# Kernel optimization log

Measured on AMD Instinct MI355X. Metric: run time of the kernel, lower is better.

The kernel has to match this reference:

```python
import jax, jax.numpy as jnp
import numpy as np

B, T = 32, 512
VOCAB, WDIM, H, NUM_LABELS = 100000, 300, 256, 2


def setup_inputs() -> dict:
    key = jax.random.key(0)
    ks = jax.random.split(key, 16)
    x = jax.random.randint(ks[0], (B, T), 0, VOCAB, dtype=jnp.int32)
    lengths = jax.random.randint(ks[1], (B,), T // 2, T + 1, dtype=jnp.int32)
    mask = (jnp.arange(T)[None, :] < lengths[:, None]).astype(jnp.int32)
    s = 0.05
    emb_table = jax.random.normal(ks[2], (VOCAB, WDIM), jnp.float32)
    W_in = jax.random.normal(ks[3], (WDIM, H), jnp.float32) * s
    b_in = jnp.zeros((H,), jnp.float32)
    Wih_f = jax.random.normal(ks[4], (H, 4 * H), jnp.float32) * s
    Whh_f = jax.random.normal(ks[5], (H, 4 * H), jnp.float32) * s
    bl_f = jnp.zeros((4 * H,), jnp.float32)
    Wih_b = jax.random.normal(ks[6], (H, 4 * H), jnp.float32) * s
    Whh_b = jax.random.normal(ks[7], (H, 4 * H), jnp.float32) * s
    bl_b = jnp.zeros((4 * H,), jnp.float32)
    Wfc = jax.random.normal(ks[8], (2 * H, H), jnp.float32) * s
    bfc = jnp.zeros((H,), jnp.float32)
    Wout = jax.random.normal(ks[9], (H, NUM_LABELS), jnp.float32) * s
    bout = jnp.zeros((NUM_LABELS,), jnp.float32)
    return dict(emb_table=emb_table, W_in=W_in, b_in=b_in,
                Wih_f=Wih_f, Whh_f=Whh_f, bl_f=bl_f,
                Wih_b=Wih_b, Whh_b=Whh_b, bl_b=bl_b,
                Wfc=Wfc, bfc=bfc, Wout=Wout, bout=bout,
                x=x, mask=mask, lengths=lengths)


def _lstm_dir(xs, maskf, Wih, Whh, b, reverse):
    # xs: [B,T,H], maskf: [B,T] float. Masked LSTM: padded steps carry state.
    xs_t = jnp.swapaxes(xs, 0, 1)                # [T,B,H]
    m_t = jnp.swapaxes(maskf, 0, 1)[..., None]   # [T,B,1]
    h0 = jnp.zeros((xs.shape[0], Whh.shape[0]), xs.dtype)
    c0 = h0

    def step(carry, inp):
        h, c = carry
        xt, mt = inp
        z = xt @ Wih + h @ Whh + b               # [B,4H]
        i, f, g, o = jnp.split(z, 4, axis=-1)
        i = jax.nn.sigmoid(i); f = jax.nn.sigmoid(f)
        g = jnp.tanh(g); o = jax.nn.sigmoid(o)
        c_new = f * c + i * g
        h_new = o * jnp.tanh(c_new)
        c = mt * c_new + (1.0 - mt) * c
        h = mt * h_new + (1.0 - mt) * h
        return (h, c), h

    _, hs = jax.lax.scan(step, (h0, c0), (xs_t, m_t), reverse=reverse)
    return jnp.swapaxes(hs, 0, 1)                # [B,T,H]


def reference(emb_table, W_in, b_in, Wih_f, Whh_f, bl_f, Wih_b, Whh_b, bl_b,
              Wfc, bfc, Wout, bout, x, mask, lengths):
    maskf = mask.astype(jnp.float32)
    x_vecs = jnp.take(emb_table, x, axis=0)          # [B,T,WDIM]
    z = jax.nn.relu(x_vecs @ W_in + b_in)            # wordvec layer + relu
    h_fwd = _lstm_dir(z, maskf, Wih_f, Whh_f, bl_f, reverse=False)
    h_bwd = _lstm_dir(z, maskf, Wih_b, Whh_b, bl_b, reverse=True)
    h_mat = jnp.concatenate([h_fwd, h_bwd], axis=-1)  # [B,T,2H]
    h_masked = h_mat * maskf[..., None]
    fc_in = jnp.sum(h_masked / lengths.astype(jnp.float32)[:, None, None], axis=1)
    fc_hidden = jax.nn.relu(fc_in @ Wfc + bfc)        # dropout = identity (eval)
    return fc_hidden @ Wout + bout                    # [B, NUM_LABELS]
```

## Files before the change

### kernel.cpp

```cpp
#include <hip/hip_runtime.h>
#include <math.h>

#define B_    32
#define T_    512
#define WDIM_ 300
#define H_    256
#define G4_   1024
#define M_    (B_ * T_)

#define NBG   16
#define NCG   4
#define NWG   128
#define THR   512
#define HXN   (2 * 2 * B_ * H_)

#define RPT4(M, b)  M(b) M((b)+1) M((b)+2) M((b)+3)
#define RPT16(M, b) RPT4(M, b) RPT4(M, (b)+4) RPT4(M, (b)+8) RPT4(M, (b)+12)
#define RPT64(M)    RPT16(M, 0) RPT16(M, 16) RPT16(M, 32) RPT16(M, 48)

__global__ __launch_bounds__(256)
void k_embed_proj(const float* __restrict__ emb, const float* __restrict__ Win,
                  const float* __restrict__ bin, const int* __restrict__ x,
                  float* __restrict__ z)
{
    __shared__ float Ash[16][132];
    __shared__ float Bsh[16][132];
    __shared__ int   rows[128];

    const int tid = threadIdx.x;
    const int tx = tid & 15, ty = tid >> 4;
    const int rm = blockIdx.y * 128;
    const int cn = blockIdx.x * 128;

    if (tid < 128) rows[tid] = x[rm + tid];
    __syncthreads();

    float acc[8][8];
#pragma unroll
    for (int i = 0; i < 8; ++i)
#pragma unroll
        for (int j = 0; j < 8; ++j) acc[i][j] = 0.f;

    for (int kc = 0; kc < 19; ++kc) {
        const int k0 = kc * 16;
#pragma unroll
        for (int e = 0; e < 8; ++e) {
            const int idx = e * 256 + tid;
            const int r = idx >> 4, kk = idx & 15;
            const int k = k0 + kk;
            const int v = rows[r];
            Ash[kk][r] = (k < WDIM_) ? emb[(size_t)v * WDIM_ + k] : 0.f;
        }
#pragma unroll
        for (int e = 0; e < 8; ++e) {
            const int idx = e * 256 + tid;
            const int kk = idx >> 7, n = idx & 127;
            const int k = k0 + kk;
            Bsh[kk][n] = (k < WDIM_) ? Win[(size_t)k * H_ + cn + n] : 0.f;
        }
        __syncthreads();
#pragma unroll
        for (int kk = 0; kk < 16; ++kk) {
            float a[8], bb[8];
#pragma unroll
            for (int i = 0; i < 8; ++i) a[i] = Ash[kk][ty * 8 + i];
#pragma unroll
            for (int j = 0; j < 8; ++j) bb[j] = Bsh[kk][tx * 8 + j];
#pragma unroll
            for (int i = 0; i < 8; ++i)
#pragma unroll
                for (int j = 0; j < 8; ++j) acc[i][j] += a[i] * bb[j];
        }
        __syncthreads();
    }

#pragma unroll
    for (int i = 0; i < 8; ++i) {
        const int row = rm + ty * 8 + i;
#pragma unroll
        for (int j = 0; j < 8; ++j) {
            const int col = cn + tx * 8 + j;
            z[(size_t)row * H_ + col] = fmaxf(acc[i][j] + bin[col], 0.f);
        }
    }
}

__global__ __launch_bounds__(256)
void k_in_proj(const float* __restrict__ z,
               const float* __restrict__ Wf, const float* __restrict__ blf,
               const float* __restrict__ Wb, const float* __restrict__ blb,
               float* __restrict__ Pf, float* __restrict__ Pb)
{
    const float* W  = blockIdx.z ? Wb  : Wf;
    const float* bl = blockIdx.z ? blb : blf;
    float*       P  = blockIdx.z ? Pb  : Pf;

    __shared__ float Ash[16][132];
    __shared__ float Bsh[16][132];

    const int tid = threadIdx.x;
    const int tx = tid & 15, ty = tid >> 4;
    const int rm = blockIdx.y * 128;
    const int cn = blockIdx.x * 128;

    float acc[8][8];
#pragma unroll
    for (int i = 0; i < 8; ++i)
#pragma unroll
        for (int j = 0; j < 8; ++j) acc[i][j] = 0.f;

    for (int kc = 0; kc < 16; ++kc) {
        const int k0 = kc * 16;
#pragma unroll
        for (int e = 0; e < 8; ++e) {
            const int idx = e * 256 + tid;
            const int r = idx >> 4, kk = idx & 15;
            Ash[kk][r] = z[(size_t)(rm + r) * H_ + k0 + kk];
        }
#pragma unroll
        for (int e = 0; e < 8; ++e) {
            const int idx = e * 256 + tid;
            const int kk = idx >> 7, n = idx & 127;
            Bsh[kk][n] = W[(size_t)(k0 + kk) * G4_ + cn + n];
        }
        __syncthreads();
#pragma unroll
        for (int kk = 0; kk < 16; ++kk) {
            float a[8], bb[8];
#pragma unroll
            for (int i = 0; i < 8; ++i) a[i] = Ash[kk][ty * 8 + i];
#pragma unroll
            for (int j = 0; j < 8; ++j) bb[j] = Bsh[kk][tx * 8 + j];
#pragma unroll
            for (int i = 0; i < 8; ++i)
#pragma unroll
                for (int j = 0; j < 8; ++j) acc[i][j] += a[i] * bb[j];
        }
        __syncthreads();
    }

#pragma unroll
    for (int i = 0; i < 8; ++i) {
        const int row = rm + ty * 8 + i;
#pragma unroll
        for (int j = 0; j < 8; ++j) {
            const int col = cn + tx * 8 + j;
            P[(size_t)row * G4_ + col] = acc[i][j] + bl[col];
        }
    }
}

__global__ void k_init(unsigned long long* __restrict__ hx)
{
    const int i = blockIdx.x * blockDim.x + threadIdx.x;
    if (i < HXN) hx[i] = 0ull;
}

__global__ __launch_bounds__(THR, 2)
void k_lstm_persist(const float* __restrict__ Pf, const float* __restrict__ Pb,
                    const float* __restrict__ Whf, const float* __restrict__ Whb,
                    const int* __restrict__ lengths,
                    unsigned long long* __restrict__ hx,
                    float* __restrict__ pool)
{
    __shared__ float h_sh[2][256];
    __shared__ float zp[4][2][256];

    const int tid = threadIdx.x;
    const int wg  = blockIdx.x;
    const int bg  = wg & 15;
    const int dir = (wg >> 4) & 1;
    const int cg  = wg >> 5;

    const float* P   = dir ? Pb  : Pf;
    const float* Whh = dir ? Whb : Whf;

    const int brow0 = bg * 2;
    const int len0 = lengths[brow0], len1 = lengths[brow0 + 1];
    const int tmax = max(len0, len1);

    const int q   = tid >> 7;
    const int c0  = (tid & 127) * 2;
    const int g0  = c0 >> 6;
    const int dd0 = c0 & 63;
    const int gcol0 = g0 * 256 + cg * 64 + dd0;
    const int q64 = q * 64;

    float2 wv[64];
    {
        const float* wp = Whh + (size_t)q64 * G4_ + gcol0;
#define LOADW(k) wv[k] = *(const float2*)(wp + (size_t)(k) * G4_);
        RPT64(LOADW)
#undef LOADW
    }

    const int gr    = tid >> 6;
    const int gdd   = tid & 63;
    const int gbrow = brow0 + gr;
    const int glen  = gr ? len1 : len0;
    float cst = 0.f, hreg = 0.f, pacc = 0.f;

    const int lrow = tid >> 8;
    const int ld   = tid & 255;
    unsigned long long* slotR = hx + ((size_t)dir * 32 + brow0 + lrow) * 256 + ld;
    unsigned long long* slotW = hx + ((size_t)dir * 32 + gbrow) * 256 + cg * 64 + gdd;
    const size_t bufStride = (size_t)2 * B_ * H_;

    for (int s = 0; s < tmax; ++s) {
        const int tt = dir ? (tmax - 1 - s) : s;

        float pv0 = 0.f, pv1 = 0.f, pv2 = 0.f, pv3 = 0.f;
        if (tid < 128) {
            const float* pr = P + (size_t)(gbrow * T_ + tt) * G4_ + cg * 64 + gdd;
            pv0 = pr[0]; pv1 = pr[256]; pv2 = pr[512]; pv3 = pr[768];
        }

        {
            const unsigned long long* sp = slotR + (size_t)(s & 1) * bufStride;
            unsigned long long pk = __hip_atomic_load(sp, __ATOMIC_RELAXED,
                                                      __HIP_MEMORY_SCOPE_AGENT);
            while ((unsigned)(pk >> 32) < (unsigned)s) {
                __builtin_amdgcn_s_sleep(1);
                pk = __hip_atomic_load(sp, __ATOMIC_RELAXED,
                                       __HIP_MEMORY_SCOPE_AGENT);
            }
            h_sh[lrow][ld] = __uint_as_float((unsigned)pk);
        }
        __syncthreads();

        {
            const float* h0 = &h_sh[0][q64];
            const float* h1 = &h_sh[1][q64];
            float a00 = 0.f, a01 = 0.f, a10 = 0.f, a11 = 0.f;
#define GEMV4(k4) { \
            const float4 hv0 = *(const float4*)(h0 + 4 * (k4)); \
            const float4 hv1 = *(const float4*)(h1 + 4 * (k4)); \
            a00 += hv0.x * wv[4*(k4)  ].x; a01 += hv0.x * wv[4*(k4)  ].y; \
            a10 += hv1.x * wv[4*(k4)  ].x; a11 += hv1.x * wv[4*(k4)  ].y; \
            a00 += hv0.y * wv[4*(k4)+1].x; a01 += hv0.y * wv[4*(k4)+1].y; \
            a10 += hv1.y * wv[4*(k4)+1].x; a11 += hv1.y * wv[4*(k4)+1].y; \
            a00 += hv0.z * wv[4*(k4)+2].x; a01 += hv0.z * wv[4*(k4)+2].y; \
            a10 += hv1.z * wv[4*(k4)+2].x; a11 += hv1.z * wv[4*(k4)+2].y; \
            a00 += hv0.w * wv[4*(k4)+3].x; a01 += hv0.w * wv[4*(k4)+3].y; \
            a10 += hv1.w * wv[4*(k4)+3].x; a11 += hv1.w * wv[4*(k4)+3].y; }
            RPT16(GEMV4, 0)
#undef GEMV4
            *(float2*)&zp[q][0][c0] = make_float2(a00, a01);
            *(float2*)&zp[q][1][c0] = make_float2(a10, a11);
        }
        __syncthreads();

        if (tid < 128) {
            const int ci = gdd;
            float zi = pv0 + zp[0][gr][ci]       + zp[1][gr][ci]       + zp[2][gr][ci]       + zp[3][gr][ci];
            float zf = pv1 + zp[0][gr][64 + ci]  + zp[1][gr][64 + ci]  + zp[2][gr][64 + ci]  + zp[3][gr][64 + ci];
            float zg = pv2 + zp[0][gr][128 + ci] + zp[1][gr][128 + ci] + zp[2][gr][128 + ci] + zp[3][gr][128 + ci];
            float zo = pv3 + zp[0][gr][192 + ci] + zp[1][gr][192 + ci] + zp[2][gr][192 + ci] + zp[3][gr][192 + ci];
            const float ig = 1.f / (1.f + expf(-zi));
            const float fg = 1.f / (1.f + expf(-zf));
            const float gg = tanhf(zg);
            const float og = 1.f / (1.f + expf(-zo));
            const float cn = fg * cst + ig * gg;
            const float hn = og * tanhf(cn);
            if (tt < glen) { cst = cn; hreg = hn; pacc += hn; }
            const unsigned long long opk =
                ((unsigned long long)(unsigned)(s + 1) << 32) |
                (unsigned long long)__float_as_uint(hreg);
            __hip_atomic_store(slotW + (size_t)((s + 1) & 1) * bufStride, opk,
                               __ATOMIC_RELAXED, __HIP_MEMORY_SCOPE_AGENT);
        }
    }

    if (tid < 128)
        pool[gbrow * 512 + dir * 256 + cg * 64 + gdd] = pacc / (float)glen;
}

__global__ __launch_bounds__(256)
void k_fc(const float* __restrict__ pool, const float* __restrict__ Wfc,
          const float* __restrict__ bfc, const float* __restrict__ Wout,
          const float* __restrict__ bout, float* __restrict__ out)
{
    __shared__ float p_sh[512];
    __shared__ float red[8];

    const int tid = threadIdx.x;
    const int b   = blockIdx.x;

    p_sh[tid]       = pool[b * 512 + tid];
    p_sh[256 + tid] = pool[b * 512 + 256 + tid];
    __syncthreads();

    float acc = bfc[tid];
#pragma unroll 8
    for (int k = 0; k < 512; ++k)
        acc += p_sh[k] * Wfc[(size_t)k * H_ + tid];
    const float fh = fmaxf(acc, 0.f);

    float p0 = fh * Wout[tid * 2 + 0];
    float p1 = fh * Wout[tid * 2 + 1];
#pragma unroll
    for (int off = 32; off > 0; off >>= 1) {
        p0 += __shfl_down(p0, off);
        p1 += __shfl_down(p1, off);
    }
    const int wave = tid >> 6;
    if ((tid & 63) == 0) { red[wave * 2] = p0; red[wave * 2 + 1] = p1; }
    __syncthreads();
    if (tid == 0) {
        out[b * 2 + 0] = red[0] + red[2] + red[4] + red[6] + bout[0];
        out[b * 2 + 1] = red[1] + red[3] + red[5] + red[7] + bout[1];
    }
}

__global__ void k_sentinel(float* out, int n)
{
    const int i = blockIdx.x * blockDim.x + threadIdx.x;
    if (i < n) out[i] = 1.0e9f;
}

extern "C" void kernel_launch(void* const* d_in, const int* in_sizes, int n_in,
                              void* d_out, int out_size, void* d_ws, size_t ws_size,
                              hipStream_t stream)
{
    const float* emb  = (const float*)d_in[0];
    const float* Win  = (const float*)d_in[1];
    const float* bin  = (const float*)d_in[2];
    const float* Wihf = (const float*)d_in[3];
    const float* Whhf = (const float*)d_in[4];
    const float* blf  = (const float*)d_in[5];
    const float* Wihb = (const float*)d_in[6];
    const float* Whhb = (const float*)d_in[7];
    const float* blb  = (const float*)d_in[8];
    const float* Wfc  = (const float*)d_in[9];
    const float* bfc  = (const float*)d_in[10];
    const float* Wout = (const float*)d_in[11];
    const float* bout = (const float*)d_in[12];
    const int*   x    = (const int*)d_in[13];
    const int*   lens = (const int*)d_in[15];
    float*       out  = (float*)d_out;

    const size_t need = ((size_t)M_ * H_ + 2 * (size_t)M_ * G4_) * sizeof(float);
    if (ws_size < need) {
        hipLaunchKernelGGL(k_sentinel, dim3(1), dim3(64), 0, stream, out, out_size);
        return;
    }

    float* z  = (float*)d_ws;
    float* Pf = z + (size_t)M_ * H_;
    float* Pb = Pf + (size_t)M_ * G4_;

    unsigned long long* hx   = (unsigned long long*)d_ws;
    float*              pool = (float*)(hx + HXN);

    hipLaunchKernelGGL(k_embed_proj, dim3(2, 128), dim3(256), 0, stream,
                       emb, Win, bin, x, z);
    hipLaunchKernelGGL(k_in_proj, dim3(8, 128, 2), dim3(256), 0, stream,
                       z, Wihf, blf, Wihb, blb, Pf, Pb);
    hipLaunchKernelGGL(k_init, dim3(128), dim3(256), 0, stream, hx);
    hipLaunchKernelGGL(k_lstm_persist, dim3(NWG), dim3(THR), 0, stream,
                       Pf, Pb, Whhf, Whhb, lens, hx, pool);
    hipLaunchKernelGGL(k_fc, dim3(32), dim3(256), 0, stream,
                       pool, Wfc, bfc, Wout, bout, out);
}
```

Baseline: 1.520 ms.

## Split LSTM hidden columns across 8 workgroups instead of 4

```diff
diff --git a/kernel.cpp b/kernel.cpp
--- a/kernel.cpp
+++ b/kernel.cpp
@@ -8,9 +8,8 @@
 #define G4_   1024
 #define M_    (B_ * T_)
 
-#define NBG   16
-#define NCG   4
-#define NWG   128
+#define NCG   8
+#define NWG   256
 #define THR   512
 #define HXN   (2 * 2 * B_ * H_)
 
@@ -164,7 +163,7 @@
                     float* __restrict__ pool)
 {
     __shared__ float h_sh[2][256];
-    __shared__ float zp[4][2][256];
+    __shared__ float zp[4][2][128];
 
     const int tid = threadIdx.x;
     const int wg  = blockIdx.x;
@@ -180,22 +179,22 @@
     const int tmax = max(len0, len1);
 
     const int q   = tid >> 7;
-    const int c0  = (tid & 127) * 2;
-    const int g0  = c0 >> 6;
-    const int dd0 = c0 & 63;
-    const int gcol0 = g0 * 256 + cg * 64 + dd0;
+    const int cl  = tid & 127;
+    const int g0  = cl >> 5;
+    const int dd0 = cl & 31;
+    const int gcol = g0 * 256 + cg * 32 + dd0;
     const int q64 = q * 64;
 
-    float2 wv[64];
+    float wv[64];
     {
-        const float* wp = Whh + (size_t)q64 * G4_ + gcol0;
-#define LOADW(k) wv[k] = *(const float2*)(wp + (size_t)(k) * G4_);
+        const float* wp = Whh + (size_t)q64 * G4_ + gcol;
+#define LOADW(k) wv[k] = wp[(size_t)(k) * G4_];
         RPT64(LOADW)
 #undef LOADW
     }
 
-    const int gr    = tid >> 6;
-    const int gdd   = tid & 63;
+    const int gr    = tid >> 5;
+    const int gd    = tid & 31;
     const int gbrow = brow0 + gr;
     const int glen  = gr ? len1 : len0;
     float cst = 0.f, hreg = 0.f, pacc = 0.f;
@@ -203,15 +202,15 @@
     const int lrow = tid >> 8;
     const int ld   = tid & 255;
     unsigned long long* slotR = hx + ((size_t)dir * 32 + brow0 + lrow) * 256 + ld;
-    unsigned long long* slotW = hx + ((size_t)dir * 32 + gbrow) * 256 + cg * 64 + gdd;
+    unsigned long long* slotW = hx + ((size_t)dir * 32 + gbrow) * 256 + cg * 32 + gd;
     const size_t bufStride = (size_t)2 * B_ * H_;
 
     for (int s = 0; s < tmax; ++s) {
         const int tt = dir ? (tmax - 1 - s) : s;
 
         float pv0 = 0.f, pv1 = 0.f, pv2 = 0.f, pv3 = 0.f;
-        if (tid < 128) {
-            const float* pr = P + (size_t)(gbrow * T_ + tt) * G4_ + cg * 64 + gdd;
+        if (tid < 64) {
+            const float* pr = P + (size_t)(gbrow * T_ + tt) * G4_ + cg * 32 + gd;
             pv0 = pr[0]; pv1 = pr[256]; pv2 = pr[512]; pv3 = pr[768];
         }
 
@@ -231,31 +230,26 @@
         {
             const float* h0 = &h_sh[0][q64];
             const float* h1 = &h_sh[1][q64];
-            float a00 = 0.f, a01 = 0.f, a10 = 0.f, a11 = 0.f;
+            float a0 = 0.f, a1 = 0.f;
 #define GEMV4(k4) { \
             const float4 hv0 = *(const float4*)(h0 + 4 * (k4)); \
             const float4 hv1 = *(const float4*)(h1 + 4 * (k4)); \
-            a00 += hv0.x * wv[4*(k4)  ].x; a01 += hv0.x * wv[4*(k4)  ].y; \
-            a10 += hv1.x * wv[4*(k4)  ].x; a11 += hv1.x * wv[4*(k4)  ].y; \
-            a00 += hv0.y * wv[4*(k4)+1].x; a01 += hv0.y * wv[4*(k4)+1].y; \
-            a10 += hv1.y * wv[4*(k4)+1].x; a11 += hv1.y * wv[4*(k4)+1].y; \
-            a00 += hv0.z * wv[4*(k4)+2].x; a01 += hv0.z * wv[4*(k4)+2].y; \
-            a10 += hv1.z * wv[4*(k4)+2].x; a11 += hv1.z * wv[4*(k4)+2].y; \
-            a00 += hv0.w * wv[4*(k4)+3].x; a01 += hv0.w * wv[4*(k4)+3].y; \
-            a10 += hv1.w * wv[4*(k4)+3].x; a11 += hv1.w * wv[4*(k4)+3].y; }
+            a0 += hv0.x * wv[4*(k4)  ]; a1 += hv1.x * wv[4*(k4)  ]; \
+            a0 += hv0.y * wv[4*(k4)+1]; a1 += hv1.y * wv[4*(k4)+1]; \
+            a0 += hv0.z * wv[4*(k4)+2]; a1 += hv1.z * wv[4*(k4)+2]; \
+            a0 += hv0.w * wv[4*(k4)+3]; a1 += hv1.w * wv[4*(k4)+3]; }
             RPT16(GEMV4, 0)
 #undef GEMV4
-            *(float2*)&zp[q][0][c0] = make_float2(a00, a01);
-            *(float2*)&zp[q][1][c0] = make_float2(a10, a11);
-        }
-        __syncthreads();
-
-        if (tid < 128) {
-            const int ci = gdd;
-            float zi = pv0 + zp[0][gr][ci]       + zp[1][gr][ci]       + zp[2][gr][ci]       + zp[3][gr][ci];
-            float zf = pv1 + zp[0][gr][64 + ci]  + zp[1][gr][64 + ci]  + zp[2][gr][64 + ci]  + zp[3][gr][64 + ci];
-            float zg = pv2 + zp[0][gr][128 + ci] + zp[1][gr][128 + ci] + zp[2][gr][128 + ci] + zp[3][gr][128 + ci];
-            float zo = pv3 + zp[0][gr][192 + ci] + zp[1][gr][192 + ci] + zp[2][gr][192 + ci] + zp[3][gr][192 + ci];
+            zp[q][0][cl] = a0;
+            zp[q][1][cl] = a1;
+        }
+        __syncthreads();
+
+        if (tid < 64) {
+            float zi = pv0 + zp[0][gr][gd]      + zp[1][gr][gd]      + zp[2][gr][gd]      + zp[3][gr][gd];
+            float zf = pv1 + zp[0][gr][32 + gd] + zp[1][gr][32 + gd] + zp[2][gr][32 + gd] + zp[3][gr][32 + gd];
+            float zg = pv2 + zp[0][gr][64 + gd] + zp[1][gr][64 + gd] + zp[2][gr][64 + gd] + zp[3][gr][64 + gd];
+            float zo = pv3 + zp[0][gr][96 + gd] + zp[1][gr][96 + gd] + zp[2][gr][96 + gd] + zp[3][gr][96 + gd];
             const float ig = 1.f / (1.f + expf(-zi));
             const float fg = 1.f / (1.f + expf(-zf));
             const float gg = tanhf(zg);
@@ -271,8 +265,8 @@
         }
     }
 
-    if (tid < 128)
-        pool[gbrow * 512 + dir * 256 + cg * 64 + gdd] = pacc / (float)glen;
+    if (tid < 64)
+        pool[gbrow * 512 + dir * 256 + cg * 32 + gd] = pacc / (float)glen;
 }
 
 __global__ __launch_bounds__(256)
```

Measured after the change: 1.380 ms. 9.2% less time.
